# Kernel optimization log

Hardware: AMD Instinct MI355X
Metric: run time of the kernel (lower is better)

Reference implementation:

```python
import math
import jax, jax.numpy as jnp
import numpy as np

B, T, D_MODEL, H, D = 2, 1024, 1024, 16, 64
NUM_LEVELS = int(math.ceil(math.log2(T + 1))) + 1  # 12 for max_seq_len=1024


def _fenwick_level(idx):
    return (idx & -idx).bit_length() - 1


def build_fenwick_masks(T, num_levels):
    """NumPy replica of the torch build_fenwick_masks; returns [L, T, T] float32."""
    j_to_nodes = {}
    for j in range(1, T + 1):
        nodes = []
        idx = j
        while idx <= T:
            nodes.append((idx, _fenwick_level(idx)))
            idx += idx & -idx
        j_to_nodes[j] = nodes
    t_to_query_nodes = {}
    for t in range(1, T + 1):
        s = set()
        idx = t
        while idx > 0:
            s.add(idx)
            idx -= idx & -idx
        t_to_query_nodes[t] = s
    masks = np.zeros((num_levels, T, T), dtype=np.float32)
    for t in range(1, T + 1):
        qn = t_to_query_nodes[t]
        for j in range(1, t + 1):
            for node_idx, node_level in j_to_nodes[j]:
                if node_idx in qn:
                    masks[min(node_level, num_levels - 1), t - 1, j - 1] = 1.0
                    break
    return masks


def setup_inputs() -> dict:
    key = jax.random.key(0)
    ks = jax.random.split(key, 8)
    s = 0.02
    return {
        "x": jax.random.normal(ks[0], (B, T, D_MODEL), jnp.float32),
        "qw": jax.random.normal(ks[1], (D_MODEL, H * D), jnp.float32) * s,
        "qb": jnp.zeros((H * D,), jnp.float32),
        "kw": jax.random.normal(ks[2], (D_MODEL, H * D), jnp.float32) * s,
        "kb": jnp.zeros((H * D,), jnp.float32),
        "vw": jax.random.normal(ks[3], (D_MODEL, H * D), jnp.float32) * s,
        "vb": jnp.zeros((H * D,), jnp.float32),
        "lw": jax.random.normal(ks[4], (D_MODEL, H * NUM_LEVELS), jnp.float32) * s,
        "lb": jnp.zeros((H * NUM_LEVELS,), jnp.float32),
        "ow": jax.random.normal(ks[5], (H * D, D_MODEL), jnp.float32) * s,
        "ob": jnp.zeros((D_MODEL,), jnp.float32),
        "level_masks": jnp.asarray(build_fenwick_masks(T, NUM_LEVELS)),
    }


def reference(x, qw, qb, kw, kb, vw, vb, lw, lb, ow, ob, level_masks):
    b, t, _ = x.shape
    phi = lambda a: jax.nn.elu(a) + 1.0  # ELU+1 feature map
    # projections -> [B, H, T, D]
    Q = (x @ qw + qb).reshape(b, t, H, D).transpose(0, 2, 1, 3)
    K = (x @ kw + kb).reshape(b, t, H, D).transpose(0, 2, 1, 3)
    V = (x @ vw + vb).reshape(b, t, H, D).transpose(0, 2, 1, 3)
    Qp, Kp = phi(Q), phi(K)
    # per-level mixing weights: [B, H, T, L]
    logits = (x @ lw + lb).reshape(b, t, H, NUM_LEVELS).transpose(0, 2, 1, 3)
    w = jax.nn.softmax(logits, axis=-1)
    # scores are level-independent in the original; compute once
    S = jnp.einsum('bhid,bhjd->bhij', Qp, Kp)
    # sum_l w_l * mask_l folded into one weighted mask: [B, H, T, T]
    Mw = jnp.einsum('bhil,lij->bhij', w, level_masks)
    Sm = S * Mw
    num = jnp.einsum('bhij,bhjd->bhid', Sm, V)
    den = jnp.maximum(jnp.sum(Sm, axis=-1, keepdims=True), 1e-6)
    out = (num / den).transpose(0, 2, 1, 3).reshape(b, t, H * D)
    return out @ ow + ob
```

## Files before the change

kernel.cpp:

```cpp
#include <hip/hip_runtime.h>
#include <math.h>

typedef __bf16 bf16;
typedef __attribute__((ext_vector_type(4))) __bf16 bf16x4;
typedef __attribute__((ext_vector_type(8))) __bf16 bf16x8;
typedef __attribute__((ext_vector_type(4))) float f32x4;

#define B_SZ 2
#define T_SZ 1024
#define DM_SZ 1024
#define H_SZ 16
#define D_SZ 64
#define L_SZ 12
#define M_ROWS 2048
#define N_PAD 3328

__device__ __forceinline__ f32x4 mfma_16x16x32(bf16x8 a, bf16x8 b, f32x4 c) {
  return __builtin_amdgcn_mfma_f32_16x16x32_bf16(a, b, c, 0, 0, 0);
}

__device__ __forceinline__ void gload_lds16(const bf16* g, bf16* l) {
  __builtin_amdgcn_global_load_lds((const __attribute__((address_space(1))) void*)g,
                                   (__attribute__((address_space(3))) void*)l,
                                   16, 0, 0);
}

__global__ __launch_bounds__(256) void k_prep(
    const float* __restrict__ x, bf16* __restrict__ xb,
    const float* __restrict__ qw, const float* __restrict__ kw,
    const float* __restrict__ vw, const float* __restrict__ ow,
    const float* __restrict__ lw,
    bf16* __restrict__ wqkvT, bf16* __restrict__ owT) {
  const int z = blockIdx.z;
  const int t = threadIdx.x;
  if (z == 5) {
    const size_t base = ((size_t)blockIdx.y * 16 + blockIdx.x) * 8192 + t * 32;
#pragma unroll
    for (int u = 0; u < 4; ++u) {
      const float* p = x + base + u * 8;
      f32x4 a = *(const f32x4*)p;
      f32x4 b = *(const f32x4*)(p + 4);
      bf16x8 o;
#pragma unroll
      for (int e = 0; e < 4; ++e) { o[e] = (bf16)a[e]; o[e + 4] = (bf16)b[e]; }
      *(bf16x8*)(xb + base + u * 8) = o;
    }
    return;
  }
  __shared__ __align__(16) bf16 tile[64][66];
  const float* in; bf16* out; int C = 1024;
  if (z == 0)      { in = qw; out = wqkvT; }
  else if (z == 1) { in = kw; out = wqkvT + (size_t)1024 * DM_SZ; }
  else if (z == 2) { in = vw; out = wqkvT + (size_t)2048 * DM_SZ; }
  else if (z == 3) { in = ow; out = owT; }
  else             { in = lw; out = wqkvT + (size_t)3072 * DM_SZ; C = 192;
                     if (blockIdx.x >= 3) return; }
  const int tc = blockIdx.x * 64;
  const int tr = blockIdx.y * 64;
  const int r = t >> 2;
  const int c4 = (t & 3) << 4;
  const float* src = in + (size_t)(tr + r) * C + tc + c4;
  f32x4 f0 = *(const f32x4*)(src);
  f32x4 f1 = *(const f32x4*)(src + 4);
  f32x4 f2 = *(const f32x4*)(src + 8);
  f32x4 f3 = *(const f32x4*)(src + 12);
#pragma unroll
  for (int e = 0; e < 4; ++e) {
    tile[r][c4 + e]      = (bf16)f0[e];
    tile[r][c4 + 4 + e]  = (bf16)f1[e];
    tile[r][c4 + 8 + e]  = (bf16)f2[e];
    tile[r][c4 + 12 + e] = (bf16)f3[e];
  }
  __syncthreads();
  bf16x8 w0, w1;
#pragma unroll
  for (int e = 0; e < 8; ++e) { w0[e] = tile[c4 + e][r]; w1[e] = tile[c4 + 8 + e][r]; }
  bf16* dst = out + (size_t)(tc + r) * DM_SZ + tr + c4;
  *(bf16x8*)(dst) = w0;
  *(bf16x8*)(dst + 8) = w1;
}

__global__ __launch_bounds__(256) void k_gemm_qkvl(
    const bf16* __restrict__ A, const bf16* __restrict__ Wt,
    const float* __restrict__ qb, const float* __restrict__ kb,
    const float* __restrict__ vb, const float* __restrict__ lb,
    bf16* __restrict__ Qp, bf16* __restrict__ Kp,
    bf16* __restrict__ VTg, float* __restrict__ logit) {
  __shared__ __align__(16) char smem[34816];
  bf16* As = (bf16*)smem;
  bf16* Bs = As + 8192;
  const int nb = blockIdx.x * 128;
  const int mb = blockIdx.y * 128;
  const int t = threadIdx.x;
  const int wv = t >> 6;
  const int lane = t & 63;
  const int l16 = lane & 15;
  const int quad = lane >> 4;
  const int wm = (wv & 1) * 64;
  const int wn = (wv >> 1) * 64;

  const int trow = t >> 3;
  const int tcol = (t & 7) * 8;

  const f32x4 zero4 = {0.f, 0.f, 0.f, 0.f};
  f32x4 acc[4][4];
#pragma unroll
  for (int i = 0; i < 4; ++i)
#pragma unroll
    for (int j = 0; j < 4; ++j) acc[i][j] = zero4;

  const bf16* ag = A + (size_t)(mb + trow) * DM_SZ + tcol;
  const bf16* bg = Wt + (size_t)(nb + trow) * DM_SZ + tcol;

  for (int k0 = 0; k0 < DM_SZ; k0 += 64) {
    __syncthreads();
#pragma unroll
    for (int i = 0; i < 4; ++i)
      gload_lds16(ag + (size_t)i * 32 * DM_SZ + k0, As + i * 2048 + t * 8);
#pragma unroll
    for (int i = 0; i < 4; ++i)
      gload_lds16(bg + (size_t)i * 32 * DM_SZ + k0, Bs + i * 2048 + t * 8);
    __syncthreads();
#pragma unroll
    for (int ks = 0; ks < 2; ++ks) {
      bf16x8 af[4];
#pragma unroll
      for (int mi = 0; mi < 4; ++mi)
        af[mi] = *(const bf16x8*)(As + (wm + mi * 16 + l16) * 64 + ks * 32 + quad * 8);
#pragma unroll
      for (int ni = 0; ni < 4; ++ni) {
        bf16x8 bfr = *(const bf16x8*)(Bs + (wn + ni * 16 + l16) * 64 + ks * 32 + quad * 8);
#pragma unroll
        for (int mi = 0; mi < 4; ++mi)
          acc[mi][ni] = mfma_16x16x32(af[mi], bfr, acc[mi][ni]);
      }
    }
  }

  const int seg = nb >> 10;
  if (seg < 2) {
    const float* bias = seg == 0 ? qb : kb;
    bf16* outp = seg == 0 ? Qp : Kp;
    const int c0 = (nb & 1023) + wn;
#pragma unroll
    for (int ni = 0; ni < 4; ++ni) {
      const int col = c0 + ni * 16 + l16;
      const float bv = bias[col];
#pragma unroll
      for (int mi = 0; mi < 4; ++mi) {
#pragma unroll
        for (int r = 0; r < 4; ++r) {
          const int row = mb + wm + mi * 16 + quad * 4 + r;
          float v = acc[mi][ni][r] + bv;
          v = (v > 0.f) ? (v + 1.f) : __expf(v);
          outp[(size_t)row * DM_SZ + col] = (bf16)v;
        }
      }
    }
  } else if (seg == 2) {
    bf16* Trt = (bf16*)smem;
    const int cb = nb - 2048;
    __syncthreads();
#pragma unroll
    for (int ni = 0; ni < 4; ++ni) {
      const int nloc = wn + ni * 16 + l16;
      const float bv = vb[cb + nloc];
#pragma unroll
      for (int mi = 0; mi < 4; ++mi) {
        const int mloc = wm + mi * 16 + quad * 4;
        bf16x4 pk;
#pragma unroll
        for (int r = 0; r < 4; ++r) pk[r] = (bf16)(acc[mi][ni][r] + bv);
        *(bf16x4*)&Trt[nloc * 136 + mloc] = pk;
      }
    }
    __syncthreads();
    const int dn = t >> 1, ch = t & 1;
    const int bq = mb >> 10;
    const int m0g = mb & 1023;
    bf16* dst = VTg + ((size_t)(bq * 1024 + cb + dn)) * T_SZ + m0g + ch * 64;
    const bf16* srcl = Trt + dn * 136 + ch * 64;
#pragma unroll
    for (int e = 0; e < 8; ++e)
      *(bf16x8*)(dst + e * 8) = *(const bf16x8*)(srcl + e * 8);
  } else {
    const int lc0 = (nb - 3072) + wn;
#pragma unroll
    for (int ni = 0; ni < 4; ++ni) {
      const int lcol = lc0 + ni * 16 + l16;
      if (lcol < H_SZ * L_SZ) {
        const float bv = lb[lcol];
#pragma unroll
        for (int mi = 0; mi < 4; ++mi) {
#pragma unroll
          for (int r = 0; r < 4; ++r) {
            const int row = mb + wm + mi * 16 + quad * 4 + r;
            logit[(size_t)row * (H_SZ * L_SZ) + lcol] = acc[mi][ni][r] + bv;
          }
        }
      }
    }
  }
}

__global__ __launch_bounds__(256) void k_attn(const bf16* __restrict__ Qp,
                                              const bf16* __restrict__ Kp,
                                              const bf16* __restrict__ VTg,
                                              const float* __restrict__ Lg,
                                              bf16* __restrict__ O) {
  __shared__ __align__(16) bf16 Ks[64][80];
  __shared__ __align__(16) bf16 VTs[64][80];
  __shared__ __align__(16) bf16 Pl[4][16][80];
  __shared__ float Ws[64 * L_SZ];

  const int idx = blockIdx.x;
  const int s = idx >> 5;
  const int bh = idx & 31;
  const int it = (s < 8) ? (15 - s) : (s - 8);
  const int b = bh >> 4;
  const int h = bh & 15;
  const int i0 = it * 64;
  const int t = threadIdx.x;
  const int wv = t >> 6;
  const int lane = t & 63;
  const int l16 = lane & 15;
  const int quad = lane >> 4;
  const int m0 = wv * 16;

  const size_t base_bt = (size_t)b * T_SZ;

  const bf16* qptr = Qp + (base_bt + i0 + m0 + l16) * DM_SZ + h * 64 + quad * 8;
  const bf16x8 aq0 = *(const bf16x8*)(qptr);
  const bf16x8 aq1 = *(const bf16x8*)(qptr + 32);

  if (t < 64) {
    const float* lp = Lg + (base_bt + i0 + t) * (H_SZ * L_SZ) + h * L_SZ;
    float v[L_SZ];
    float m = -1e30f;
#pragma unroll
    for (int l = 0; l < L_SZ; ++l) { v[l] = lp[l]; m = fmaxf(m, v[l]); }
    float sum = 0.f;
#pragma unroll
    for (int l = 0; l < L_SZ; ++l) { v[l] = __expf(v[l] - m); sum += v[l]; }
    const float inv = 1.f / sum;
#pragma unroll
    for (int l = 0; l < L_SZ; ++l) Ws[t * L_SZ + l] = v[l] * inv;
  }

  const f32x4 zero4 = {0.f, 0.f, 0.f, 0.f};
  f32x4 accn[4];
#pragma unroll
  for (int tn = 0; tn < 4; ++tn) accn[tn] = zero4;
  float den[4] = {0.f, 0.f, 0.f, 0.f};

  const int sr = t >> 2;
  const int sc = (t & 3) << 4;
  const int il_base = m0 + quad * 4;

  const bf16* vtrow = VTg + ((size_t)bh * 64 + sr) * T_SZ;

  for (int jt = 0; jt <= it; ++jt) {
    const int j0 = jt * 64;
    const bf16* kpg = Kp + (base_bt + j0 + sr) * DM_SZ + h * 64 + sc;
    bf16x8 k0v = *(const bf16x8*)(kpg);
    bf16x8 k1v = *(const bf16x8*)(kpg + 8);
    const bf16* vpg = vtrow + j0 + sc;
    bf16x8 v0v = *(const bf16x8*)(vpg);
    bf16x8 v1v = *(const bf16x8*)(vpg + 8);
    __syncthreads();
    *(bf16x8*)&Ks[sr][sc] = k0v;
    *(bf16x8*)&Ks[sr][sc + 8] = k1v;
    *(bf16x8*)&VTs[sr][sc] = v0v;
    *(bf16x8*)&VTs[sr][sc + 8] = v1v;
    __syncthreads();

    f32x4 sacc[4];
#pragma unroll
    for (int tn = 0; tn < 4; ++tn) {
      sacc[tn] = zero4;
      bf16x8 bk0 = *(const bf16x8*)&Ks[tn * 16 + l16][quad * 8];
      bf16x8 bk1 = *(const bf16x8*)&Ks[tn * 16 + l16][32 + quad * 8];
      sacc[tn] = mfma_16x16x32(aq0, bk0, sacc[tn]);
      sacc[tn] = mfma_16x16x32(aq1, bk1, sacc[tn]);
    }

    if (jt < it) {
      const int lvlA = 6 + (31 - __clz((unsigned)(it ^ jt)));
      const int lvlB = 6 + (31 - __clz((unsigned)((it + 1) ^ jt)));
      float wrow[4];
#pragma unroll
      for (int r = 0; r < 4; ++r) {
        const int il = il_base + r;
        wrow[r] = Ws[il * L_SZ + ((il == 63) ? lvlB : lvlA)];
      }
#pragma unroll
      for (int tn = 0; tn < 4; ++tn) {
#pragma unroll
        for (int r = 0; r < 4; ++r) {
          const float p = sacc[tn][r] * wrow[r];
          den[r] += p;
          Pl[wv][quad * 4 + r][(tn * 16 + l16) ^ (quad << 4)] = (bf16)p;
        }
      }
    } else {
#pragma unroll
      for (int tn = 0; tn < 4; ++tn) {
#pragma unroll
        for (int r = 0; r < 4; ++r) {
          const int il = il_base + r;
          const int ig = i0 + il;
          const int jg = j0 + tn * 16 + l16;
          float p = 0.f;
          if (jg <= ig) {
            const int lvl = 31 - __clz((unsigned)((ig + 1) ^ jg));
            p = sacc[tn][r] * Ws[il * L_SZ + lvl];
          }
          den[r] += p;
          Pl[wv][quad * 4 + r][(tn * 16 + l16) ^ (quad << 4)] = (bf16)p;
        }
      }
    }

#pragma unroll
    for (int ks = 0; ks < 2; ++ks) {
      bf16x8 apf = *(const bf16x8*)&Pl[wv][l16][(ks * 32 + quad * 8) ^ ((l16 >> 2) << 4)];
#pragma unroll
      for (int tn = 0; tn < 4; ++tn) {
        bf16x8 bvf = *(const bf16x8*)&VTs[tn * 16 + l16][ks * 32 + quad * 8];
        accn[tn] = mfma_16x16x32(apf, bvf, accn[tn]);
      }
    }
  }

#pragma unroll
  for (int r = 0; r < 4; ++r) {
    float d = den[r];
    d += __shfl_xor(d, 1, 64);
    d += __shfl_xor(d, 2, 64);
    d += __shfl_xor(d, 4, 64);
    d += __shfl_xor(d, 8, 64);
    den[r] = fmaxf(d, 1e-6f);
  }

#pragma unroll
  for (int tn = 0; tn < 4; ++tn) {
#pragma unroll
    for (int r = 0; r < 4; ++r) {
      const int il = il_base + r;
      O[(base_bt + i0 + il) * DM_SZ + h * 64 + tn * 16 + l16] =
          (bf16)(accn[tn][r] / den[r]);
    }
  }
}

__global__ __launch_bounds__(256) void k_gemm_out(const bf16* __restrict__ A,
                                                  const bf16* __restrict__ Wt,
                                                  const float* __restrict__ ob,
                                                  float* __restrict__ out) {
  __shared__ __align__(16) bf16 As[64 * 64];
  __shared__ __align__(16) bf16 Bs[64 * 64];
  const int nb = blockIdx.x * 64;
  const int mb = blockIdx.y * 64;
  const int t = threadIdx.x;
  const int wv = t >> 6;
  const int lane = t & 63;
  const int l16 = lane & 15;
  const int quad = lane >> 4;
  const int wm = wv * 16;

  const int trow = t >> 3;
  const int tcol = (t & 7) * 8;

  const f32x4 zero4 = {0.f, 0.f, 0.f, 0.f};
  f32x4 acc[4];
#pragma unroll
  for (int j = 0; j < 4; ++j) acc[j] = zero4;

  const bf16* ag = A + (size_t)(mb + trow) * DM_SZ + tcol;
  const bf16* bg = Wt + (size_t)(nb + trow) * DM_SZ + tcol;

  for (int k0 = 0; k0 < DM_SZ; k0 += 64) {
    __syncthreads();
    gload_lds16(ag + k0, As + t * 8);
    gload_lds16(ag + (size_t)32 * DM_SZ + k0, As + 2048 + t * 8);
    gload_lds16(bg + k0, Bs + t * 8);
    gload_lds16(bg + (size_t)32 * DM_SZ + k0, Bs + 2048 + t * 8);
    __syncthreads();
#pragma unroll
    for (int ks = 0; ks < 2; ++ks) {
      bf16x8 af = *(const bf16x8*)(As + (wm + l16) * 64 + ks * 32 + quad * 8);
#pragma unroll
      for (int ni = 0; ni < 4; ++ni) {
        bf16x8 bfr = *(const bf16x8*)(Bs + (ni * 16 + l16) * 64 + ks * 32 + quad * 8);
        acc[ni] = mfma_16x16x32(af, bfr, acc[ni]);
      }
    }
  }
#pragma unroll
  for (int ni = 0; ni < 4; ++ni) {
    const int col = nb + ni * 16 + l16;
    const float bv = ob[col];
#pragma unroll
    for (int r = 0; r < 4; ++r) {
      const int row = mb + wm + quad * 4 + r;
      out[(size_t)row * DM_SZ + col] = acc[ni][r] + bv;
    }
  }
}

extern "C" void kernel_launch(void* const* d_in, const int* in_sizes, int n_in,
                              void* d_out, int out_size, void* d_ws, size_t ws_size,
                              hipStream_t stream) {
  (void)in_sizes; (void)n_in; (void)out_size; (void)ws_size;
  const float* x  = (const float*)d_in[0];
  const float* qw = (const float*)d_in[1];
  const float* qb = (const float*)d_in[2];
  const float* kw = (const float*)d_in[3];
  const float* kb = (const float*)d_in[4];
  const float* vw = (const float*)d_in[5];
  const float* vb = (const float*)d_in[6];
  const float* lw = (const float*)d_in[7];
  const float* lb = (const float*)d_in[8];
  const float* ow = (const float*)d_in[9];
  const float* ob = (const float*)d_in[10];

  char* ws = (char*)d_ws;
  size_t off = 0;
  auto alloc = [&](size_t bytes) -> char* {
    char* p = ws + off;
    off += (bytes + 255) & ~(size_t)255;
    return p;
  };
  bf16* xb     = (bf16*)alloc((size_t)M_ROWS * DM_SZ * 2);
  bf16* wqkvT  = (bf16*)alloc((size_t)N_PAD * DM_SZ * 2);
  bf16* owT    = (bf16*)alloc((size_t)DM_SZ * DM_SZ * 2);
  bf16* Qp     = (bf16*)alloc((size_t)M_ROWS * DM_SZ * 2);
  bf16* Kpb    = (bf16*)alloc((size_t)M_ROWS * DM_SZ * 2);
  bf16* VTg    = (bf16*)alloc((size_t)M_ROWS * DM_SZ * 2);
  bf16* attn   = (bf16*)alloc((size_t)M_ROWS * DM_SZ * 2);
  float* logit = (float*)alloc((size_t)M_ROWS * H_SZ * L_SZ * 4);

  const dim3 blk(256);
  k_prep<<<dim3(16, 16, 6), blk, 0, stream>>>(x, xb, qw, kw, vw, ow, lw, wqkvT, owT);
  k_gemm_qkvl<<<dim3(N_PAD / 128, M_ROWS / 128), blk, 0, stream>>>(
      xb, wqkvT, qb, kb, vb, lb, Qp, Kpb, VTg, logit);
  k_attn<<<dim3((T_SZ / 64) * B_SZ * H_SZ), blk, 0, stream>>>(Qp, Kpb, VTg, logit, attn);
  k_gemm_out<<<dim3(DM_SZ / 64, M_ROWS / 64), blk, 0, stream>>>(attn, owT, ob, (float*)d_out);
}
```

Measured before the change: 182.0 us.

## Double-buffer K/V and GEMM tiles with async global-to-LDS loads

The attention kernel now stages K and V^T tiles into two swizzled LDS buffers using direct global-to-LDS loads. The next tile is prefetched while the current one is consumed, replacing the register round-trip and the two barriers per iteration with a single barrier. The output GEMM gets the same double-buffered async staging, and the MFMA sections are wrapped in s_setprio. The cost is more LDS per block, which may lower occupancy, and correctness now relies on the barrier draining the outstanding async loads.

```diff
diff --git a/kernel.cpp b/kernel.cpp
--- a/kernel.cpp
+++ b/kernel.cpp
@@ -208,8 +208,8 @@
                                               const bf16* __restrict__ VTg,
                                               const float* __restrict__ Lg,
                                               bf16* __restrict__ O) {
-  __shared__ __align__(16) bf16 Ks[64][80];
-  __shared__ __align__(16) bf16 VTs[64][80];
+  __shared__ __align__(16) bf16 Ks[2][64 * 64];
+  __shared__ __align__(16) bf16 VTs[2][64 * 64];
   __shared__ __align__(16) bf16 Pl[4][16][80];
   __shared__ float Ws[64 * L_SZ];
 
@@ -229,6 +229,24 @@
 
   const size_t base_bt = (size_t)b * T_SZ;
 
+  const int st_r0  = wv * 16 + (lane >> 3);
+  const int st_cs  = (((lane & 7) ^ (lane >> 3)) << 3);
+  const int st_lds = wv * 1024 + lane * 8;
+  const bf16* kbase = Kp + (base_bt + st_r0) * DM_SZ + h * 64 + st_cs;
+  const bf16* vbase = VTg + ((size_t)bh * 64 + st_r0) * T_SZ + st_cs;
+
+  auto stage = [&](int jt, int buf) {
+    const int j0s = jt * 64;
+    const bf16* kg = kbase + (size_t)j0s * DM_SZ;
+    gload_lds16(kg, &Ks[buf][st_lds]);
+    gload_lds16(kg + (size_t)8 * DM_SZ, &Ks[buf][st_lds + 512]);
+    const bf16* vg = vbase + j0s;
+    gload_lds16(vg, &VTs[buf][st_lds]);
+    gload_lds16(vg + (size_t)8 * T_SZ, &VTs[buf][st_lds + 512]);
+  };
+
+  stage(0, 0);
+
   const bf16* qptr = Qp + (base_bt + i0 + m0 + l16) * DM_SZ + h * 64 + quad * 8;
   const bf16x8 aq0 = *(const bf16x8*)(qptr);
   const bf16x8 aq1 = *(const bf16x8*)(qptr + 32);
@@ -253,37 +271,28 @@
   for (int tn = 0; tn < 4; ++tn) accn[tn] = zero4;
   float den[4] = {0.f, 0.f, 0.f, 0.f};
 
-  const int sr = t >> 2;
-  const int sc = (t & 3) << 4;
   const int il_base = m0 + quad * 4;
-
-  const bf16* vtrow = VTg + ((size_t)bh * 64 + sr) * T_SZ;
+  const int rsw = (l16 & 7) << 3;
 
   for (int jt = 0; jt <= it; ++jt) {
-    const int j0 = jt * 64;
-    const bf16* kpg = Kp + (base_bt + j0 + sr) * DM_SZ + h * 64 + sc;
-    bf16x8 k0v = *(const bf16x8*)(kpg);
-    bf16x8 k1v = *(const bf16x8*)(kpg + 8);
-    const bf16* vpg = vtrow + j0 + sc;
-    bf16x8 v0v = *(const bf16x8*)(vpg);
-    bf16x8 v1v = *(const bf16x8*)(vpg + 8);
-    __syncthreads();
-    *(bf16x8*)&Ks[sr][sc] = k0v;
-    *(bf16x8*)&Ks[sr][sc + 8] = k1v;
-    *(bf16x8*)&VTs[sr][sc] = v0v;
-    *(bf16x8*)&VTs[sr][sc + 8] = v1v;
-    __syncthreads();
+    const int cur = jt & 1;
+    __syncthreads();
+    if (jt < it) stage(jt + 1, cur ^ 1);
 
     f32x4 sacc[4];
+    __builtin_amdgcn_s_setprio(1);
 #pragma unroll
     for (int tn = 0; tn < 4; ++tn) {
       sacc[tn] = zero4;
-      bf16x8 bk0 = *(const bf16x8*)&Ks[tn * 16 + l16][quad * 8];
-      bf16x8 bk1 = *(const bf16x8*)&Ks[tn * 16 + l16][32 + quad * 8];
+      const int rb = (tn * 16 + l16) * 64;
+      bf16x8 bk0 = *(const bf16x8*)&Ks[cur][rb + ((quad * 8) ^ rsw)];
+      bf16x8 bk1 = *(const bf16x8*)&Ks[cur][rb + ((32 + quad * 8) ^ rsw)];
       sacc[tn] = mfma_16x16x32(aq0, bk0, sacc[tn]);
       sacc[tn] = mfma_16x16x32(aq1, bk1, sacc[tn]);
     }
-
+    __builtin_amdgcn_s_setprio(0);
+
+    const int j0 = jt * 64;
     if (jt < it) {
       const int lvlA = 6 + (31 - __clz((unsigned)(it ^ jt)));
       const int lvlB = 6 + (31 - __clz((unsigned)((it + 1) ^ jt)));
@@ -321,15 +330,18 @@
       }
     }
 
+    __builtin_amdgcn_s_setprio(1);
 #pragma unroll
     for (int ks = 0; ks < 2; ++ks) {
       bf16x8 apf = *(const bf16x8*)&Pl[wv][l16][(ks * 32 + quad * 8) ^ ((l16 >> 2) << 4)];
 #pragma unroll
       for (int tn = 0; tn < 4; ++tn) {
-        bf16x8 bvf = *(const bf16x8*)&VTs[tn * 16 + l16][ks * 32 + quad * 8];
+        bf16x8 bvf = *(const bf16x8*)&VTs[cur][(tn * 16 + l16) * 64 +
+                                              ((ks * 32 + quad * 8) ^ rsw)];
         accn[tn] = mfma_16x16x32(apf, bvf, accn[tn]);
       }
     }
+    __builtin_amdgcn_s_setprio(0);
   }
 
 #pragma unroll
@@ -357,8 +369,8 @@
                                                   const bf16* __restrict__ Wt,
                                                   const float* __restrict__ ob,
                                                   float* __restrict__ out) {
-  __shared__ __align__(16) bf16 As[64 * 64];
-  __shared__ __align__(16) bf16 Bs[64 * 64];
+  __shared__ __align__(16) bf16 As[2][64 * 64];
+  __shared__ __align__(16) bf16 Bs[2][64 * 64];
   const int nb = blockIdx.x * 64;
   const int mb = blockIdx.y * 64;
   const int t = threadIdx.x;
@@ -379,19 +391,24 @@
   const bf16* ag = A + (size_t)(mb + trow) * DM_SZ + tcol;
   const bf16* bg = Wt + (size_t)(nb + trow) * DM_SZ + tcol;
 
+  auto stageg = [&](int k0, int buf) {
+    gload_lds16(ag + k0, As[buf] + t * 8);
+    gload_lds16(ag + (size_t)32 * DM_SZ + k0, As[buf] + 2048 + t * 8);
+    gload_lds16(bg + k0, Bs[buf] + t * 8);
+    gload_lds16(bg + (size_t)32 * DM_SZ + k0, Bs[buf] + 2048 + t * 8);
+  };
+
+  stageg(0, 0);
   for (int k0 = 0; k0 < DM_SZ; k0 += 64) {
-    __syncthreads();
-    gload_lds16(ag + k0, As + t * 8);
-    gload_lds16(ag + (size_t)32 * DM_SZ + k0, As + 2048 + t * 8);
-    gload_lds16(bg + k0, Bs + t * 8);
-    gload_lds16(bg + (size_t)32 * DM_SZ + k0, Bs + 2048 + t * 8);
-    __syncthreads();
+    const int cur = (k0 >> 6) & 1;
+    __syncthreads();
+    if (k0 + 64 < DM_SZ) stageg(k0 + 64, cur ^ 1);
 #pragma unroll
     for (int ks = 0; ks < 2; ++ks) {
-      bf16x8 af = *(const bf16x8*)(As + (wm + l16) * 64 + ks * 32 + quad * 8);
+      bf16x8 af = *(const bf16x8*)(As[cur] + (wm + l16) * 64 + ks * 32 + quad * 8);
 #pragma unroll
       for (int ni = 0; ni < 4; ++ni) {
-        bf16x8 bfr = *(const bf16x8*)(Bs + (ni * 16 + l16) * 64 + ks * 32 + quad * 8);
+        bf16x8 bfr = *(const bf16x8*)(Bs[cur] + (ni * 16 + l16) * 64 + ks * 32 + quad * 8);
         acc[ni] = mfma_16x16x32(af, bfr, acc[ni]);
       }
     }
```

Measured after the change: 184.5 us. About the same (+1.3%).
